# Kernel tuning notes

Measured on AMD Instinct MI355X. Metric: run time of the kernel, lower is better.

Reference implementation:

```python
import jax, jax.numpy as jnp
import numpy as np

B, FIN, N, E = 4, 354, 4096, 65536
HID, HEADS, PH = 352, 4, 88  # per_head = gat_hidden // num_heads
EPS = 1e-5
NEG_SLOPE = 0.2  # GATConv leaky_relu slope


def setup_inputs() -> dict:
    key = jax.random.key(0)
    ks = jax.random.split(key, 32)
    s = 0.05
    inp = {
        "x": jax.random.normal(ks[0], (B, FIN, N), dtype=jnp.float32),
        "edge_index": jax.random.randint(ks[1], (2, E), 0, N, dtype=jnp.int32),
        # GATConv 1: in=354 -> heads*per_head=352
        "W1": jax.random.normal(ks[2], (FIN, HID), dtype=jnp.float32) * s,
        "att_src1": jax.random.normal(ks[3], (HEADS, PH), dtype=jnp.float32) * s,
        "att_dst1": jax.random.normal(ks[4], (HEADS, PH), dtype=jnp.float32) * s,
        "b1": jnp.zeros((HID,), jnp.float32),
        "gn1_w": jnp.ones((HID,), jnp.float32),
        "gn1_b": jnp.zeros((HID,), jnp.float32),
        "gn1_ms": jnp.ones((HID,), jnp.float32),
        # GATConv 2
        "W2": jax.random.normal(ks[5], (HID, HID), dtype=jnp.float32) * s,
        "att_src2": jax.random.normal(ks[6], (HEADS, PH), dtype=jnp.float32) * s,
        "att_dst2": jax.random.normal(ks[7], (HEADS, PH), dtype=jnp.float32) * s,
        "b2": jnp.zeros((HID,), jnp.float32),
        "gn2_w": jnp.ones((HID,), jnp.float32),
        "gn2_b": jnp.zeros((HID,), jnp.float32),
        "gn2_ms": jnp.ones((HID,), jnp.float32),
        # GATConv 3
        "W3": jax.random.normal(ks[8], (HID, HID), dtype=jnp.float32) * s,
        "att_src3": jax.random.normal(ks[9], (HEADS, PH), dtype=jnp.float32) * s,
        "att_dst3": jax.random.normal(ks[10], (HEADS, PH), dtype=jnp.float32) * s,
        "b3": jnp.zeros((HID,), jnp.float32),
        "gn3_w": jnp.ones((HID,), jnp.float32),
        "gn3_b": jnp.zeros((HID,), jnp.float32),
        "gn3_ms": jnp.ones((HID,), jnp.float32),
        # classifier Linear(352 -> 1)
        "clf_w": jax.random.normal(ks[11], (1, HID), dtype=jnp.float32) * s,
        "clf_b": jnp.zeros((1,), jnp.float32),
    }
    return inp


def reference(x, edge_index, W1, att_src1, att_dst1, b1, gn1_w, gn1_b, gn1_ms,
              W2, att_src2, att_dst2, b2, gn2_w, gn2_b, gn2_ms,
              W3, att_src3, att_dst3, b3, gn3_w, gn3_b, gn3_ms,
              clf_w, clf_b):
    n = x.shape[2]
    h_in = jnp.transpose(x, (0, 2, 1))  # [B, N, FIN]
    # PyG GATConv default add_self_loops=True
    loop = jnp.arange(n, dtype=edge_index.dtype)
    src = jnp.concatenate([edge_index[0], loop])
    dst = jnp.concatenate([edge_index[1], loop])

    def gat(h, W, a_s, a_d, b):  # h: [N, Fin]
        H, C = a_s.shape
        xh = (h @ W).reshape(n, H, C)                      # [N, H, C]
        a_src = jnp.sum(xh * a_s, axis=-1)                 # [N, H]
        a_dst = jnp.sum(xh * a_d, axis=-1)                 # [N, H]
        logits = jax.nn.leaky_relu(a_src[src] + a_dst[dst], NEG_SLOPE)  # [Etot, H]
        m = jax.ops.segment_max(logits, dst, num_segments=n)
        ex = jnp.exp(logits - m[dst])
        den = jax.ops.segment_sum(ex, dst, num_segments=n)
        alpha = ex / den[dst]                              # segment softmax over in-edges
        out = jax.ops.segment_sum(xh[src] * alpha[:, :, None], dst, num_segments=n)
        return out.reshape(n, H * C) + b

    def gnorm(h, w, b, ms):  # GraphNorm over a single graph
        mu = jnp.mean(h, axis=0)
        o = h - ms * mu
        var = jnp.mean(o * o, axis=0)
        return o / jnp.sqrt(var + EPS) * w + b

    def per_graph(h):
        h1 = jax.nn.relu(gnorm(gat(h, W1, att_src1, att_dst1, b1), gn1_w, gn1_b, gn1_ms))
        h2 = jax.nn.relu(gnorm(gat(h1, W2, att_src2, att_dst2, b2), gn2_w, gn2_b, gn2_ms) + h1)
        h3 = jax.nn.relu(gnorm(gat(h2, W3, att_src3, att_dst3, b3), gn3_w, gn3_b, gn3_ms) + h2)
        return jnp.mean(h3, axis=0)  # global_mean_pool

    pooled = jax.vmap(per_graph)(h_in)  # [B, HID]
    return pooled @ clf_w.T + clf_b     # [B, 1]
```

## Files before the change

### kernel.cpp

```cpp
#include <hip/hip_runtime.h>
#include <math.h>

#define N_NODES 4096
#define B_GR 4
#define FIN_K 354
#define K1P 384
#define HID 352
#define NHEAD 4
#define PH 88
#define E_EDGES 65536
#define ETOT (E_EDGES + N_NODES)
#define EPSV 1e-5f
#define SLOPE 0.2f
#define SPLITS 64

typedef unsigned short u16;
typedef unsigned int u32;
typedef __attribute__((ext_vector_type(8))) short bf16x8;
typedef __attribute__((ext_vector_type(4))) float f32x4;

__device__ __forceinline__ void split_bf16(float v, u16& hi, u16& lo) {
    u32 u = __float_as_uint(v);
    hi = (u16)(u >> 16);
    float rem = v - __uint_as_float(((u32)hi) << 16);
    lo = (u16)(__float_as_uint(rem) >> 16);
}

__device__ __forceinline__ u16 bf16_rne(float v) {
    u32 u = __float_as_uint(v);
    u32 r = u + 0x7FFFu + ((u >> 16) & 1u);
    return (u16)(r >> 16);
}

__global__ void k_zero_int(int* p, int n) {
    int i = blockIdx.x * blockDim.x + threadIdx.x;
    if (i < n) p[i] = 0;
}

__global__ void k_hist(const int* __restrict__ ei, int* __restrict__ cnt) {
    int e = blockIdx.x * blockDim.x + threadIdx.x;
    if (e >= ETOT) return;
    int dst = (e < E_EDGES) ? ei[E_EDGES + e] : (e - E_EDGES);
    atomicAdd(&cnt[dst], 1);
}

__global__ void k_scan(const int* __restrict__ cnt, int* __restrict__ rp) {
    __shared__ int tot[256];
    int t = threadIdx.x;
    int base = t * 16;
    int loc[16];
    int s = 0;
    #pragma unroll
    for (int i = 0; i < 16; i++) { loc[i] = s; s += cnt[base + i]; }
    tot[t] = s;
    __syncthreads();
    for (int off = 1; off < 256; off <<= 1) {
        int v = (t >= off) ? tot[t - off] : 0;
        __syncthreads();
        tot[t] += v;
        __syncthreads();
    }
    int excl = (t == 0) ? 0 : tot[t - 1];
    #pragma unroll
    for (int i = 0; i < 16; i++) rp[base + i] = excl + loc[i];
    if (t == 255) rp[N_NODES] = tot[255];
}

__global__ void k_scatter(const int* __restrict__ ei, const int* __restrict__ rp,
                          int* __restrict__ cur, int* __restrict__ col) {
    int e = blockIdx.x * blockDim.x + threadIdx.x;
    if (e >= ETOT) return;
    int src, dst;
    if (e < E_EDGES) { src = ei[e]; dst = ei[E_EDGES + e]; }
    else { src = e - E_EDGES; dst = src; }
    int pos = rp[dst] + atomicAdd(&cur[dst], 1);
    col[pos] = src;
}

__global__ __launch_bounds__(256) void k_prep_x(const float* __restrict__ x,
                                                u16* __restrict__ xth, u16* __restrict__ xtl) {
    __shared__ float tile[64][65];
    int b = blockIdx.z;
    int n0 = blockIdx.x * 64;
    int k0 = blockIdx.y * 64;
    int tid = threadIdx.x;
    int r = tid >> 2;
    int cq = (tid & 3) * 16;
    int kglob = k0 + r;
    if (kglob < FIN_K) {
        const float* src = x + ((size_t)b * FIN_K + kglob) * N_NODES + n0 + cq;
        float4 v0 = *reinterpret_cast<const float4*>(src + 0);
        float4 v1 = *reinterpret_cast<const float4*>(src + 4);
        float4 v2 = *reinterpret_cast<const float4*>(src + 8);
        float4 v3 = *reinterpret_cast<const float4*>(src + 12);
        *reinterpret_cast<float4*>(&tile[r][cq + 0]) = v0;
        *reinterpret_cast<float4*>(&tile[r][cq + 4]) = v1;
        *reinterpret_cast<float4*>(&tile[r][cq + 8]) = v2;
        *reinterpret_cast<float4*>(&tile[r][cq + 12]) = v3;
    } else {
        float4 z = make_float4(0.f, 0.f, 0.f, 0.f);
        *reinterpret_cast<float4*>(&tile[r][cq + 0]) = z;
        *reinterpret_cast<float4*>(&tile[r][cq + 4]) = z;
        *reinterpret_cast<float4*>(&tile[r][cq + 8]) = z;
        *reinterpret_cast<float4*>(&tile[r][cq + 12]) = z;
    }
    __syncthreads();
    int nr = tid >> 2;
    int kq = (tid & 3) * 16;
    u16 hb[16], lb[16];
    #pragma unroll
    for (int i = 0; i < 16; i++) split_bf16(tile[kq + i][nr], hb[i], lb[i]);
    size_t o = ((size_t)b * N_NODES + n0 + nr) * K1P + k0 + kq;
    *reinterpret_cast<uint4*>(xth + o)     = *reinterpret_cast<uint4*>(hb);
    *reinterpret_cast<uint4*>(xth + o + 8) = *reinterpret_cast<uint4*>(hb + 8);
    *reinterpret_cast<uint4*>(xtl + o)     = *reinterpret_cast<uint4*>(lb);
    *reinterpret_cast<uint4*>(xtl + o + 8) = *reinterpret_cast<uint4*>(lb + 8);
}

__global__ void k_prep_w(const float* __restrict__ W, u16* __restrict__ wth, u16* __restrict__ wtl,
                         int K, int KP) {
    int n = blockIdx.x;
    for (int k = threadIdx.x; k < KP; k += 64) {
        float v = 0.f;
        if (n < HID && k < K) v = W[(size_t)k * HID + n];
        u16 hi, lo;
        split_bf16(v, hi, lo);
        wth[(size_t)n * KP + k] = hi;
        wtl[(size_t)n * KP + k] = lo;
    }
}

__global__ __launch_bounds__(256) void k_gemm_mfma(
    const u16* __restrict__ Ah, const u16* __restrict__ Al,
    const u16* __restrict__ Bh, const u16* __restrict__ Bl,
    float* __restrict__ C, int K)
{
    __shared__ __align__(16) char smem[24576];
    const int AHo = 0, ALo = 4096, BHo = 8192, BLo = 16384;
    int b = blockIdx.z;
    int m0 = blockIdx.y * 64;
    int n0 = blockIdx.x * 128;
    int tid = threadIdx.x;
    int lane = tid & 63, wid = tid >> 6;
    int wr = (wid >> 1) * 32, wc = (wid & 1) * 64;
    int lrow = lane & 15, kgv = lane >> 4;

    const u16* Abh = Ah + (size_t)b * N_NODES * K;
    const u16* Abl = Al + (size_t)b * N_NODES * K;

    int srow = tid >> 2, skg = tid & 3;
    int sxor = (srow >> 1) & 3;
    int st_lds = srow * 64 + ((skg ^ sxor) << 4);
    int st_lds1 = (srow + 64) * 64 + ((skg ^ sxor) << 4);
    size_t a_g  = (size_t)(m0 + srow) * K + skg * 8;
    size_t b_g0 = (size_t)(n0 + srow) * K + skg * 8;
    size_t b_g1 = (size_t)(n0 + srow + 64) * K + skg * 8;

    int a_ad[2], b_ad[4];
    #pragma unroll
    for (int mf = 0; mf < 2; mf++) {
        int r = wr + mf * 16 + lrow;
        a_ad[mf] = r * 64 + ((kgv ^ ((r >> 1) & 3)) << 4);
    }
    #pragma unroll
    for (int nf = 0; nf < 4; nf++) {
        int c = wc + nf * 16 + lrow;
        b_ad[nf] = c * 64 + ((kgv ^ ((c >> 1) & 3)) << 4);
    }

    f32x4 acc[2][4];
    #pragma unroll
    for (int i = 0; i < 2; i++)
        #pragma unroll
        for (int j = 0; j < 4; j++) acc[i][j] = (f32x4){0.f, 0.f, 0.f, 0.f};

    uint4 cah = *(const uint4*)(Abh + a_g);
    uint4 cal = *(const uint4*)(Abl + a_g);
    uint4 cbh0 = *(const uint4*)(Bh + b_g0);
    uint4 cbl0 = *(const uint4*)(Bl + b_g0);
    uint4 cbh1 = *(const uint4*)(Bh + b_g1);
    uint4 cbl1 = *(const uint4*)(Bl + b_g1);

    for (int k0 = 0; k0 < K; k0 += 32) {
        __syncthreads();
        *(uint4*)(smem + AHo + st_lds) = cah;
        *(uint4*)(smem + ALo + st_lds) = cal;
        *(uint4*)(smem + BHo + st_lds) = cbh0;
        *(uint4*)(smem + BLo + st_lds) = cbl0;
        *(uint4*)(smem + BHo + st_lds1) = cbh1;
        *(uint4*)(smem + BLo + st_lds1) = cbl1;
        int k1 = k0 + 32;
        uint4 nah, nal, nbh0, nbl0, nbh1, nbl1;
        bool more = k1 < K;
        if (more) {
            nah = *(const uint4*)(Abh + a_g + k1);
            nal = *(const uint4*)(Abl + a_g + k1);
            nbh0 = *(const uint4*)(Bh + b_g0 + k1);
            nbl0 = *(const uint4*)(Bl + b_g0 + k1);
            nbh1 = *(const uint4*)(Bh + b_g1 + k1);
            nbl1 = *(const uint4*)(Bl + b_g1 + k1);
        }
        __syncthreads();

        bf16x8 fah0 = *(const bf16x8*)(smem + AHo + a_ad[0]);
        bf16x8 fah1 = *(const bf16x8*)(smem + AHo + a_ad[1]);
        bf16x8 fal0 = *(const bf16x8*)(smem + ALo + a_ad[0]);
        bf16x8 fal1 = *(const bf16x8*)(smem + ALo + a_ad[1]);
        #pragma unroll
        for (int nf = 0; nf < 4; nf++) {
            bf16x8 fbh = *(const bf16x8*)(smem + BHo + b_ad[nf]);
            bf16x8 fbl = *(const bf16x8*)(smem + BLo + b_ad[nf]);
            acc[0][nf] = __builtin_amdgcn_mfma_f32_16x16x32_bf16(fah0, fbh, acc[0][nf], 0, 0, 0);
            acc[1][nf] = __builtin_amdgcn_mfma_f32_16x16x32_bf16(fah1, fbh, acc[1][nf], 0, 0, 0);
            acc[0][nf] = __builtin_amdgcn_mfma_f32_16x16x32_bf16(fal0, fbh, acc[0][nf], 0, 0, 0);
            acc[1][nf] = __builtin_amdgcn_mfma_f32_16x16x32_bf16(fal1, fbh, acc[1][nf], 0, 0, 0);
            acc[0][nf] = __builtin_amdgcn_mfma_f32_16x16x32_bf16(fah0, fbl, acc[0][nf], 0, 0, 0);
            acc[1][nf] = __builtin_amdgcn_mfma_f32_16x16x32_bf16(fah1, fbl, acc[1][nf], 0, 0, 0);
        }
        if (more) { cah = nah; cal = nal; cbh0 = nbh0; cbl0 = nbl0; cbh1 = nbh1; cbl1 = nbl1; }
    }

    #pragma unroll
    for (int nf = 0; nf < 4; nf++) {
        int colg = n0 + wc + nf * 16 + lrow;
        if (colg < HID) {
            #pragma unroll
            for (int mf = 0; mf < 2; mf++) {
                #pragma unroll
                for (int r = 0; r < 4; r++) {
                    int rowg = m0 + wr + mf * 16 + kgv * 4 + r;
                    C[((size_t)b * N_NODES + rowg) * HID + colg] = acc[mf][nf][r];
                }
            }
        }
    }
}

__global__ void k_att(const float* __restrict__ xh,
                      const float* __restrict__ as_, const float* __restrict__ ad_,
                      float* __restrict__ osrc, float* __restrict__ odst,
                      u16* __restrict__ xb16) {
    int idx = blockIdx.x * blockDim.x + threadIdx.x;
    if (idx >= B_GR * N_NODES * NHEAD) return;
    int h = idx & 3;
    int bn = idx >> 2;
    const float* base = xh + (size_t)bn * HID + h * PH;
    const float* a1 = as_ + h * PH;
    const float* a2 = ad_ + h * PH;
    float s1 = 0.f, s2 = 0.f;
    u16 packed[PH];
    #pragma unroll
    for (int c = 0; c < PH; c += 4) {
        float4 v = *reinterpret_cast<const float4*>(&base[c]);
        float4 w1 = *reinterpret_cast<const float4*>(&a1[c]);
        float4 w2 = *reinterpret_cast<const float4*>(&a2[c]);
        s1 += v.x * w1.x + v.y * w1.y + v.z * w1.z + v.w * w1.w;
        s2 += v.x * w2.x + v.y * w2.y + v.z * w2.z + v.w * w2.w;
        packed[c + 0] = bf16_rne(v.x);
        packed[c + 1] = bf16_rne(v.y);
        packed[c + 2] = bf16_rne(v.z);
        packed[c + 3] = bf16_rne(v.w);
    }
    osrc[idx] = s1;
    odst[idx] = s2;
    u16* dstp = xb16 + (size_t)idx * PH;
    #pragma unroll
    for (int i = 0; i < PH; i += 8)
        *reinterpret_cast<uint4*>(dstp + i) = *reinterpret_cast<uint4*>(packed + i);
}

__global__ __launch_bounds__(256) void k_agg(
    const u16* __restrict__ xb16, const float* __restrict__ asrc,
    const float* __restrict__ adst, const int* __restrict__ rp,
    const int* __restrict__ col, const float* __restrict__ bias,
    float* __restrict__ g)
{
    int id = blockIdx.x;
    int xcd = id & 7;
    int gr = xcd >> 1;
    int w = threadIdx.x >> 6;
    int l = threadIdx.x & 63;
    int dst = ((((id >> 3) << 1) | (xcd & 1)) << 2) + w;
    int h = l & 3, slot = l >> 2;
    int beg = rp[dst];
    int deg = rp[dst + 1] - beg;
    const float* asG = asrc + (size_t)gr * N_NODES * NHEAD;
    float my_adst = adst[((size_t)gr * N_NODES + dst) * 4 + h];
    const u32* xb = reinterpret_cast<const u32*>(xb16) + (size_t)gr * N_NODES * 176;

    int c1 = l + 64, c2 = l + 128;
    int hh0 = l / 44, hh1 = c1 / 44, hh2 = c2 / 44;
    bool has2 = (l < 48);
    float2 a0 = {0.f, 0.f}, a1 = {0.f, 0.f}, a2 = {0.f, 0.f};
    float den = 0.f;

    for (int c0 = 0; c0 < deg; c0 += 16) {
        int nthis = min(16, deg - c0);
        int sIdx = col[beg + c0 + ((slot < nthis) ? slot : 0)];
        float xv = asG[sIdx * 4 + h] + my_adst;
        float lg = (xv > 0.f) ? xv : SLOPE * xv;
        float e = (slot < nthis) ? expf(lg) : 0.f;
        den += e;
        int off = sIdx * 176;
        #pragma unroll 2
        for (int i = 0; i < nthis; i++) {
            int offi = __shfl(off, i << 2);
            float e0 = __shfl(e, (i << 2) | hh0);
            float e1 = __shfl(e, (i << 2) | hh1);
            u32 v0 = xb[offi + l];
            u32 v1 = xb[offi + c1];
            a0.x = fmaf(e0, __uint_as_float(v0 << 16), a0.x);
            a0.y = fmaf(e0, __uint_as_float(v0 & 0xFFFF0000u), a0.y);
            a1.x = fmaf(e1, __uint_as_float(v1 << 16), a1.x);
            a1.y = fmaf(e1, __uint_as_float(v1 & 0xFFFF0000u), a1.y);
            if (has2) {
                float e2 = __shfl(e, (i << 2) | hh2);
                u32 v2 = xb[offi + c2];
                a2.x = fmaf(e2, __uint_as_float(v2 << 16), a2.x);
                a2.y = fmaf(e2, __uint_as_float(v2 & 0xFFFF0000u), a2.y);
            }
        }
    }

    den += __shfl_xor(den, 4);
    den += __shfl_xor(den, 8);
    den += __shfl_xor(den, 16);
    den += __shfl_xor(den, 32);
    float inv = 1.0f / den;
    float i0 = __shfl(inv, hh0);
    float i1 = __shfl(inv, hh1);
    float* grow = g + ((size_t)gr * N_NODES + dst) * HID;
    float2 b0 = *reinterpret_cast<const float2*>(bias + 2 * l);
    float2 b1 = *reinterpret_cast<const float2*>(bias + 2 * c1);
    float2 o0 = {a0.x * i0 + b0.x, a0.y * i0 + b0.y};
    float2 o1 = {a1.x * i1 + b1.x, a1.y * i1 + b1.y};
    *reinterpret_cast<float2*>(grow + 2 * l) = o0;
    *reinterpret_cast<float2*>(grow + 2 * c1) = o1;
    if (has2) {
        float i2 = __shfl(inv, hh2);
        float2 b2 = *reinterpret_cast<const float2*>(bias + 2 * c2);
        float2 o2 = {a2.x * i2 + b2.x, a2.y * i2 + b2.y};
        *reinterpret_cast<float2*>(grow + 2 * c2) = o2;
    }
}

__global__ __launch_bounds__(384) void k_reduce(const float* __restrict__ g,
                                                float* __restrict__ ps, float* __restrict__ pss) {
    int b = blockIdx.y, chunk = blockIdx.x;
    int c = threadIdx.x;
    if (c >= HID) return;
    const int ROWS = N_NODES / SPLITS;
    int n0 = chunk * ROWS;
    const float* base = g + ((size_t)b * N_NODES + n0) * HID + c;
    float s = 0.f, ss = 0.f;
    for (int r = 0; r < ROWS; r++) {
        float v = base[(size_t)r * HID];
        s += v;
        ss = fmaf(v, v, ss);
    }
    ps[((size_t)b * SPLITS + chunk) * HID + c] = s;
    pss[((size_t)b * SPLITS + chunk) * HID + c] = ss;
}

__global__ void k_norm_final(const float* __restrict__ ps, const float* __restrict__ pss,
                             const float* __restrict__ ms, const float* __restrict__ w,
                             float* __restrict__ mu_ms, float* __restrict__ scale) {
    int b = blockIdx.x;
    int c = threadIdx.x;
    if (c >= HID) return;
    float s = 0.f, ss = 0.f;
    for (int q = 0; q < SPLITS; q++) {
        s += ps[((size_t)b * SPLITS + q) * HID + c];
        ss += pss[((size_t)b * SPLITS + q) * HID + c];
    }
    float mu = s / (float)N_NODES;
    float Eh2 = ss / (float)N_NODES;
    float msv = ms[c];
    float var = Eh2 - 2.f * msv * mu * mu + msv * msv * mu * mu;
    float rstd = 1.0f / sqrtf(var + EPSV);
    mu_ms[b * HID + c] = msv * mu;
    scale[b * HID + c] = rstd * w[c];
}

template<bool RES, bool WBF>
__global__ void k_apply(const float* __restrict__ g, const float* __restrict__ hprev,
                        const float* __restrict__ mu_ms, const float* __restrict__ scale,
                        const float* __restrict__ gnb, float* __restrict__ hout,
                        u16* __restrict__ hh, u16* __restrict__ hl) {
    size_t idx = (size_t)blockIdx.x * blockDim.x + threadIdx.x;
    size_t total = (size_t)B_GR * N_NODES * HID;
    if (idx >= total) return;
    int c = (int)(idx % HID);
    int b = (int)(idx / ((size_t)N_NODES * HID));
    float v = g[idx];
    float o = (v - mu_ms[b * HID + c]) * scale[b * HID + c] + gnb[c];
    if (RES) o += hprev[idx];
    o = fmaxf(o, 0.f);
    hout[idx] = o;
    if (WBF) {
        u16 hi, lo;
        split_bf16(o, hi, lo);
        hh[idx] = hi;
        hl[idx] = lo;
    }
}

__global__ __launch_bounds__(384) void k_final(const float* __restrict__ ps,
                                               const float* __restrict__ clfw,
                                               const float* __restrict__ clfb,
                                               float* __restrict__ out) {
    int b = blockIdx.x;
    int t = threadIdx.x;
    __shared__ float buf[384];
    float v = 0.f;
    if (t < HID) {
        float s = 0.f;
        for (int q = 0; q < SPLITS; q++) s += ps[((size_t)b * SPLITS + q) * HID + t];
        v = (s / (float)N_NODES) * clfw[t];
    }
    buf[t] = v;
    __syncthreads();
    if (t < 64) {
        float acc = 0.f;
        for (int j = t; j < 384; j += 64) acc += buf[j];
        for (int off = 32; off; off >>= 1) acc += __shfl_down(acc, off);
        if (t == 0) out[b] = acc + clfb[0];
    }
}

extern "C" void kernel_launch(void* const* d_in, const int* in_sizes, int n_in,
                              void* d_out, int out_size, void* d_ws, size_t ws_size,
                              hipStream_t stream) {
    const float* x = (const float*)d_in[0];
    const int* ei = (const int*)d_in[1];
    const float* W[3]   = {(const float*)d_in[2],  (const float*)d_in[9],  (const float*)d_in[16]};
    const float* as_[3] = {(const float*)d_in[3],  (const float*)d_in[10], (const float*)d_in[17]};
    const float* ad_[3] = {(const float*)d_in[4],  (const float*)d_in[11], (const float*)d_in[18]};
    const float* bi[3]  = {(const float*)d_in[5],  (const float*)d_in[12], (const float*)d_in[19]};
    const float* gw[3]  = {(const float*)d_in[6],  (const float*)d_in[13], (const float*)d_in[20]};
    const float* gb[3]  = {(const float*)d_in[7],  (const float*)d_in[14], (const float*)d_in[21]};
    const float* gms[3] = {(const float*)d_in[8],  (const float*)d_in[15], (const float*)d_in[22]};
    const float* clfw = (const float*)d_in[23];
    const float* clfb = (const float*)d_in[24];
    float* out = (float*)d_out;

    char* ws = (char*)d_ws;
    size_t off = 0;
    auto alloc = [&](size_t bytes) -> void* {
        void* p = ws + off;
        off += (bytes + 255) & ~(size_t)255;
        return p;
    };
    size_t bigf = sizeof(float) * (size_t)B_GR * N_NODES * HID;
    float* xh    = (float*)alloc(bigf);
    float* gbuf  = xh;
    float* hA    = (float*)alloc(bigf);
    float* hB    = (float*)alloc(bigf);
    size_t bfbytes = sizeof(u16) * (size_t)B_GR * N_NODES * K1P;
    u16* bf_hi = (u16*)alloc(bfbytes);
    u16* bf_lo = (u16*)alloc(bfbytes);
    u16* xb16  = (u16*)alloc(sizeof(u16) * (size_t)B_GR * N_NODES * NHEAD * PH);
    u16* wt_h[3]; u16* wt_l[3];
    wt_h[0] = (u16*)alloc(sizeof(u16) * 384 * K1P);
    wt_l[0] = (u16*)alloc(sizeof(u16) * 384 * K1P);
    for (int l = 1; l < 3; l++) {
        wt_h[l] = (u16*)alloc(sizeof(u16) * 384 * HID);
        wt_l[l] = (u16*)alloc(sizeof(u16) * 384 * HID);
    }
    float* a_s   = (float*)alloc(sizeof(float) * B_GR * N_NODES * NHEAD);
    float* a_d   = (float*)alloc(sizeof(float) * B_GR * N_NODES * NHEAD);
    float* ps    = (float*)alloc(sizeof(float) * B_GR * SPLITS * HID);
    float* pss   = (float*)alloc(sizeof(float) * B_GR * SPLITS * HID);
    float* mu_ms = (float*)alloc(sizeof(float) * B_GR * HID);
    float* scale = (float*)alloc(sizeof(float) * B_GR * HID);
    int* rp  = (int*)alloc(sizeof(int) * (N_NODES + 1));
    int* cnt = (int*)alloc(sizeof(int) * N_NODES);
    int* col = (int*)alloc(sizeof(int) * ETOT);

    k_prep_w<<<384, 64, 0, stream>>>(W[0], wt_h[0], wt_l[0], FIN_K, K1P);
    k_prep_w<<<384, 64, 0, stream>>>(W[1], wt_h[1], wt_l[1], HID, HID);
    k_prep_w<<<384, 64, 0, stream>>>(W[2], wt_h[2], wt_l[2], HID, HID);
    k_prep_x<<<dim3(64, 6, B_GR), 256, 0, stream>>>(x, bf_hi, bf_lo);

    k_zero_int<<<(N_NODES + 255) / 256, 256, 0, stream>>>(cnt, N_NODES);
    k_hist<<<(ETOT + 255) / 256, 256, 0, stream>>>(ei, cnt);
    k_scan<<<1, 256, 0, stream>>>(cnt, rp);
    k_zero_int<<<(N_NODES + 255) / 256, 256, 0, stream>>>(cnt, N_NODES);
    k_scatter<<<(ETOT + 255) / 256, 256, 0, stream>>>(ei, rp, cnt, col);

    const float* hin = nullptr;
    float* hcur = hA;
    dim3 ggrid(3, N_NODES / 64, B_GR);
    dim3 rgrid(SPLITS, B_GR);
    size_t total = (size_t)B_GR * N_NODES * HID;
    int ablocks = (int)((total + 255) / 256);

    for (int l = 0; l < 3; l++) {
        int K = (l == 0) ? K1P : HID;
        k_gemm_mfma<<<ggrid, 256, 0, stream>>>(bf_hi, bf_lo, wt_h[l], wt_l[l], xh, K);
        k_att<<<(B_GR * N_NODES * NHEAD + 255) / 256, 256, 0, stream>>>(xh, as_[l], ad_[l], a_s, a_d, xb16);
        k_agg<<<B_GR * N_NODES / 4, 256, 0, stream>>>(xb16, a_s, a_d, rp, col, bi[l], gbuf);
        k_reduce<<<rgrid, 384, 0, stream>>>(gbuf, ps, pss);
        k_norm_final<<<B_GR, 384, 0, stream>>>(ps, pss, gms[l], gw[l], mu_ms, scale);
        if (l == 0)      k_apply<false, true ><<<ablocks, 256, 0, stream>>>(gbuf, nullptr, mu_ms, scale, gb[l], hcur, bf_hi, bf_lo);
        else if (l == 1) k_apply<true,  true ><<<ablocks, 256, 0, stream>>>(gbuf, hin, mu_ms, scale, gb[l], hcur, bf_hi, bf_lo);
        else             k_apply<true,  false><<<ablocks, 256, 0, stream>>>(gbuf, hin, mu_ms, scale, gb[l], hcur, bf_hi, bf_lo);
        hin = hcur;
        hcur = (hcur == hA) ? hB : hA;
    }
    k_reduce<<<rgrid, 384, 0, stream>>>(hin, ps, pss);
    k_final<<<B_GR, 384, 0, stream>>>(ps, clfw, clfb, out);
}
```

Before: 319.3 us.

## Fold attention projections into GEMM as extra columns and drop fp32 intermediates

Precomputes W·att_src and W·att_dst per head and appends them as 8 extra output columns of the augmented weight, so the GEMM directly emits per-node attention scores. The GEMM epilogue now writes bf16 features straight into the aggregation buffer, and the separate attention kernel and the fp32 xh write/read go away. The apply kernel is vectorised to two elements per thread and reads the residual from the hi/lo bf16 split buffers instead of an fp32 copy; it writes fp32 output only on the last layer. This trades some precision in the attention logits (computed via the bf16-split GEMM on combined weights) for less memory traffic and one fewer launch per layer.

```diff
diff --git a/kernel.cpp b/kernel.cpp
--- a/kernel.cpp
+++ b/kernel.cpp
@@ -130,10 +130,39 @@
     }
 }
 
+__global__ void k_prep_waug(const float* __restrict__ W,
+                            const float* __restrict__ as_, const float* __restrict__ ad_,
+                            u16* __restrict__ wth, u16* __restrict__ wtl, int K, int KP) {
+    int k = blockIdx.x * 64 + threadIdx.x;
+    if (k >= KP) return;
+    float accs[4] = {0.f, 0.f, 0.f, 0.f}, accd[4] = {0.f, 0.f, 0.f, 0.f};
+    if (k < K) {
+        const float* wrow = W + (size_t)k * HID;
+        for (int h = 0; h < 4; h++) {
+            float ss = 0.f, sd = 0.f;
+            for (int j = 0; j < PH; j++) {
+                float w = wrow[h * PH + j];
+                ss = fmaf(w, as_[h * PH + j], ss);
+                sd = fmaf(w, ad_[h * PH + j], sd);
+            }
+            accs[h] = ss; accd[h] = sd;
+        }
+    }
+    for (int h = 0; h < 4; h++) {
+        u16 hi, lo;
+        split_bf16(accs[h], hi, lo);
+        wth[(size_t)(352 + h) * KP + k] = hi;
+        wtl[(size_t)(352 + h) * KP + k] = lo;
+        split_bf16(accd[h], hi, lo);
+        wth[(size_t)(356 + h) * KP + k] = hi;
+        wtl[(size_t)(356 + h) * KP + k] = lo;
+    }
+}
+
 __global__ __launch_bounds__(256) void k_gemm_mfma(
     const u16* __restrict__ Ah, const u16* __restrict__ Al,
     const u16* __restrict__ Bh, const u16* __restrict__ Bl,
-    float* __restrict__ C, int K)
+    u16* __restrict__ xb16, float* __restrict__ a_s, float* __restrict__ a_d, int K)
 {
     __shared__ __align__(16) char smem[24576];
     const int AHo = 0, ALo = 4096, BHo = 8192, BLo = 16384;
@@ -229,44 +258,23 @@
                 #pragma unroll
                 for (int r = 0; r < 4; r++) {
                     int rowg = m0 + wr + mf * 16 + kgv * 4 + r;
-                    C[((size_t)b * N_NODES + rowg) * HID + colg] = acc[mf][nf][r];
+                    xb16[((size_t)b * N_NODES + rowg) * HID + colg] = bf16_rne(acc[mf][nf][r]);
+                }
+            }
+        } else if (colg < 360) {
+            int which = colg - 352;
+            float* dbuf = (which < 4) ? a_s : a_d;
+            int hsel = which & 3;
+            #pragma unroll
+            for (int mf = 0; mf < 2; mf++) {
+                #pragma unroll
+                for (int r = 0; r < 4; r++) {
+                    int rowg = m0 + wr + mf * 16 + kgv * 4 + r;
+                    dbuf[((size_t)b * N_NODES + rowg) * 4 + hsel] = acc[mf][nf][r];
                 }
             }
         }
     }
-}
-
-__global__ void k_att(const float* __restrict__ xh,
-                      const float* __restrict__ as_, const float* __restrict__ ad_,
-                      float* __restrict__ osrc, float* __restrict__ odst,
-                      u16* __restrict__ xb16) {
-    int idx = blockIdx.x * blockDim.x + threadIdx.x;
-    if (idx >= B_GR * N_NODES * NHEAD) return;
-    int h = idx & 3;
-    int bn = idx >> 2;
-    const float* base = xh + (size_t)bn * HID + h * PH;
-    const float* a1 = as_ + h * PH;
-    const float* a2 = ad_ + h * PH;
-    float s1 = 0.f, s2 = 0.f;
-    u16 packed[PH];
-    #pragma unroll
-    for (int c = 0; c < PH; c += 4) {
-        float4 v = *reinterpret_cast<const float4*>(&base[c]);
-        float4 w1 = *reinterpret_cast<const float4*>(&a1[c]);
-        float4 w2 = *reinterpret_cast<const float4*>(&a2[c]);
-        s1 += v.x * w1.x + v.y * w1.y + v.z * w1.z + v.w * w1.w;
-        s2 += v.x * w2.x + v.y * w2.y + v.z * w2.z + v.w * w2.w;
-        packed[c + 0] = bf16_rne(v.x);
-        packed[c + 1] = bf16_rne(v.y);
-        packed[c + 2] = bf16_rne(v.z);
-        packed[c + 3] = bf16_rne(v.w);
-    }
-    osrc[idx] = s1;
-    odst[idx] = s2;
-    u16* dstp = xb16 + (size_t)idx * PH;
-    #pragma unroll
-    for (int i = 0; i < PH; i += 8)
-        *reinterpret_cast<uint4*>(dstp + i) = *reinterpret_cast<uint4*>(packed + i);
 }
 
 __global__ __launch_bounds__(256) void k_agg(
@@ -382,26 +390,38 @@
     scale[b * HID + c] = rstd * w[c];
 }
 
-template<bool RES, bool WBF>
-__global__ void k_apply(const float* __restrict__ g, const float* __restrict__ hprev,
+template<bool RES, bool WBF, bool WOUT>
+__global__ void k_apply(const float* __restrict__ g,
                         const float* __restrict__ mu_ms, const float* __restrict__ scale,
                         const float* __restrict__ gnb, float* __restrict__ hout,
                         u16* __restrict__ hh, u16* __restrict__ hl) {
-    size_t idx = (size_t)blockIdx.x * blockDim.x + threadIdx.x;
-    size_t total = (size_t)B_GR * N_NODES * HID;
-    if (idx >= total) return;
-    int c = (int)(idx % HID);
-    int b = (int)(idx / ((size_t)N_NODES * HID));
-    float v = g[idx];
-    float o = (v - mu_ms[b * HID + c]) * scale[b * HID + c] + gnb[c];
-    if (RES) o += hprev[idx];
-    o = fmaxf(o, 0.f);
-    hout[idx] = o;
+    size_t i2 = (size_t)blockIdx.x * blockDim.x + threadIdx.x;
+    size_t total2 = (size_t)B_GR * N_NODES * HID / 2;
+    if (i2 >= total2) return;
+    size_t e = i2 * 2;
+    int c = (int)(e % HID);
+    int b = (int)(e / ((size_t)N_NODES * HID));
+    float2 v = *reinterpret_cast<const float2*>(g + e);
+    float2 mm = *reinterpret_cast<const float2*>(mu_ms + b * HID + c);
+    float2 sc = *reinterpret_cast<const float2*>(scale + b * HID + c);
+    float2 gb2 = *reinterpret_cast<const float2*>(gnb + c);
+    float o0 = (v.x - mm.x) * sc.x + gb2.x;
+    float o1 = (v.y - mm.y) * sc.y + gb2.y;
+    if (RES) {
+        u32 ph = *reinterpret_cast<const u32*>(hh + e);
+        u32 pl = *reinterpret_cast<const u32*>(hl + e);
+        o0 += __uint_as_float((ph & 0xFFFFu) << 16) + __uint_as_float((pl & 0xFFFFu) << 16);
+        o1 += __uint_as_float(ph & 0xFFFF0000u) + __uint_as_float(pl & 0xFFFF0000u);
+    }
+    o0 = fmaxf(o0, 0.f);
+    o1 = fmaxf(o1, 0.f);
+    if (WOUT) *reinterpret_cast<float2*>(hout + e) = make_float2(o0, o1);
     if (WBF) {
-        u16 hi, lo;
-        split_bf16(o, hi, lo);
-        hh[idx] = hi;
-        hl[idx] = lo;
+        u16 h0, l0, h1, l1;
+        split_bf16(o0, h0, l0);
+        split_bf16(o1, h1, l1);
+        *reinterpret_cast<u32*>(hh + e) = (u32)h0 | ((u32)h1 << 16);
+        *reinterpret_cast<u32*>(hl + e) = (u32)l0 | ((u32)l1 << 16);
     }
 }
 
@@ -452,10 +472,8 @@
         return p;
     };
     size_t bigf = sizeof(float) * (size_t)B_GR * N_NODES * HID;
-    float* xh    = (float*)alloc(bigf);
-    float* gbuf  = xh;
+    float* gbuf  = (float*)alloc(bigf);
     float* hA    = (float*)alloc(bigf);
-    float* hB    = (float*)alloc(bigf);
     size_t bfbytes = sizeof(u16) * (size_t)B_GR * N_NODES * K1P;
     u16* bf_hi = (u16*)alloc(bfbytes);
     u16* bf_lo = (u16*)alloc(bfbytes);
@@ -480,6 +498,9 @@
     k_prep_w<<<384, 64, 0, stream>>>(W[0], wt_h[0], wt_l[0], FIN_K, K1P);
     k_prep_w<<<384, 64, 0, stream>>>(W[1], wt_h[1], wt_l[1], HID, HID);
     k_prep_w<<<384, 64, 0, stream>>>(W[2], wt_h[2], wt_l[2], HID, HID);
+    k_prep_waug<<<(K1P + 63) / 64, 64, 0, stream>>>(W[0], as_[0], ad_[0], wt_h[0], wt_l[0], FIN_K, K1P);
+    k_prep_waug<<<(HID + 63) / 64, 64, 0, stream>>>(W[1], as_[1], ad_[1], wt_h[1], wt_l[1], HID, HID);
+    k_prep_waug<<<(HID + 63) / 64, 64, 0, stream>>>(W[2], as_[2], ad_[2], wt_h[2], wt_l[2], HID, HID);
     k_prep_x<<<dim3(64, 6, B_GR), 256, 0, stream>>>(x, bf_hi, bf_lo);
 
     k_zero_int<<<(N_NODES + 255) / 256, 256, 0, stream>>>(cnt, N_NODES);
@@ -488,26 +509,21 @@
     k_zero_int<<<(N_NODES + 255) / 256, 256, 0, stream>>>(cnt, N_NODES);
     k_scatter<<<(ETOT + 255) / 256, 256, 0, stream>>>(ei, rp, cnt, col);
 
-    const float* hin = nullptr;
-    float* hcur = hA;
     dim3 ggrid(3, N_NODES / 64, B_GR);
     dim3 rgrid(SPLITS, B_GR);
-    size_t total = (size_t)B_GR * N_NODES * HID;
-    int ablocks = (int)((total + 255) / 256);
+    size_t total2 = (size_t)B_GR * N_NODES * HID / 2;
+    int ablocks = (int)((total2 + 255) / 256);
 
     for (int l = 0; l < 3; l++) {
         int K = (l == 0) ? K1P : HID;
-        k_gemm_mfma<<<ggrid, 256, 0, stream>>>(bf_hi, bf_lo, wt_h[l], wt_l[l], xh, K);
-        k_att<<<(B_GR * N_NODES * NHEAD + 255) / 256, 256, 0, stream>>>(xh, as_[l], ad_[l], a_s, a_d, xb16);
+        k_gemm_mfma<<<ggrid, 256, 0, stream>>>(bf_hi, bf_lo, wt_h[l], wt_l[l], xb16, a_s, a_d, K);
         k_agg<<<B_GR * N_NODES / 4, 256, 0, stream>>>(xb16, a_s, a_d, rp, col, bi[l], gbuf);
         k_reduce<<<rgrid, 384, 0, stream>>>(gbuf, ps, pss);
         k_norm_final<<<B_GR, 384, 0, stream>>>(ps, pss, gms[l], gw[l], mu_ms, scale);
-        if (l == 0)      k_apply<false, true ><<<ablocks, 256, 0, stream>>>(gbuf, nullptr, mu_ms, scale, gb[l], hcur, bf_hi, bf_lo);
-        else if (l == 1) k_apply<true,  true ><<<ablocks, 256, 0, stream>>>(gbuf, hin, mu_ms, scale, gb[l], hcur, bf_hi, bf_lo);
-        else             k_apply<true,  false><<<ablocks, 256, 0, stream>>>(gbuf, hin, mu_ms, scale, gb[l], hcur, bf_hi, bf_lo);
-        hin = hcur;
-        hcur = (hcur == hA) ? hB : hA;
-    }
-    k_reduce<<<rgrid, 384, 0, stream>>>(hin, ps, pss);
+        if (l == 0)      k_apply<false, true,  false><<<ablocks, 256, 0, stream>>>(gbuf, mu_ms, scale, gb[l], hA, bf_hi, bf_lo);
+        else if (l == 1) k_apply<true,  true,  false><<<ablocks, 256, 0, stream>>>(gbuf, mu_ms, scale, gb[l], hA, bf_hi, bf_lo);
+        else             k_apply<true,  false, true ><<<ablocks, 256, 0, stream>>>(gbuf, mu_ms, scale, gb[l], hA, bf_hi, bf_lo);
+    }
+    k_reduce<<<rgrid, 384, 0, stream>>>(hA, ps, pss);
     k_final<<<B_GR, 384, 0, stream>>>(ps, clfw, clfb, out);
 }
```

Result: faster. 310.2 us (-2.9%).
